# Kernel tuning notes

Measured on AMD Instinct MI355X. Metric: run time of the kernel, lower is better.

The kernel has to match this reference:

```python
import jax, jax.numpy as jnp
import numpy as np

HIDDEN = 64

def setup_inputs() -> dict:
    key = jax.random.key(0)
    ks = jax.random.split(key, 10)
    B, E = 8, 200000
    h = jax.random.normal(ks[0], (B, E, HIDDEN), dtype=jnp.float32)
    J = jax.random.normal(ks[1], (B, E, 1), dtype=jnp.float32)
    b_in = jax.random.normal(ks[2], (B, E, 1), dtype=jnp.float32)
    b_out = jax.random.normal(ks[3], (B, E, 1), dtype=jnp.float32)
    d_in = HIDDEN + 4
    # PyTorch Linear default init: U(-1/sqrt(fan_in), 1/sqrt(fan_in))
    def lin(kw, kb, fan_in, fan_out):
        bound = 1.0 / np.sqrt(fan_in)
        W = jax.random.uniform(kw, (fan_in, fan_out), minval=-bound, maxval=bound, dtype=jnp.float32)
        b = jax.random.uniform(kb, (fan_out,), minval=-bound, maxval=bound, dtype=jnp.float32)
        return W, b
    W1, b1 = lin(ks[4], ks[5], d_in, 64)
    W2, b2 = lin(ks[6], ks[7], 64, 64)
    W3, b3 = lin(ks[8], ks[9], 64, 5)
    return {"h": h, "J": J, "b_in": b_in, "b_out": b_out,
            "W1": W1, "b1": b1, "W2": W2, "b2": b2, "W3": W3, "b3": b3}

def reference(h, J, b_in, b_out, W1, b1, W2, b2, W3, b3):
    # concat order matches torch.cat((h, b_in, b_out, J, -J), 2)
    x = jnp.concatenate((h, b_in, b_out, J, -J), axis=2)  # [B,E,hidden+4]
    x = jax.nn.relu(jnp.einsum('bei,io->beo', x, W1) + b1)
    x = jax.nn.relu(jnp.einsum('bei,io->beo', x, W2) + b2)
    message = jnp.einsum('bei,io->beo', x, W3) + b3  # [B,E,5]
    return message
```

## Files before the change

### kernel.cpp

```cpp
#include <hip/hip_runtime.h>

typedef __bf16 bf16x8 __attribute__((ext_vector_type(8)));
typedef float  f32x4  __attribute__((ext_vector_type(4)));

typedef const void GV __attribute__((address_space(1)));
typedef void       LV __attribute__((address_space(3)));

#define MFMA(A, B, C) __builtin_amdgcn_mfma_f32_16x16x32_bf16((A), (B), (C), 0, 0, 0)
#define GLL(gp, lp) __builtin_amdgcn_global_load_lds((GV*)(gp), (LV*)(lp), 16, 0, 0)

__global__ __launch_bounds__(256, 2)
void msg_mlp(const float* __restrict__ hbuf, const float* __restrict__ Jbuf,
             const float* __restrict__ binb, const float* __restrict__ boutb,
             const float* __restrict__ W1, const float* __restrict__ b1,
             const float* __restrict__ W2, const float* __restrict__ b2,
             const float* __restrict__ W3, const float* __restrict__ b3,
             float* __restrict__ out, int n_rows, int n_tiles)
{
    __shared__ __align__(16) char smem[32768];
    const int lane = threadIdx.x & 63;
    const int e = lane & 15;
    const int q = lane >> 4;
    const int wv = (int)(threadIdx.x >> 6);
    const int wid = blockIdx.x * 4 + wv;
    const int nw  = gridDim.x * 4;
    char* wbase = smem + wv * 8192;

    const int o_e = 16 * (lane ^ q);
    const int o_o = 16 * (lane ^ (q + 4));
    const int X   = (e & 7) << 4;
    const int d0 = 256*e + ((64*q +  0) ^ X);
    const int d1 = 256*e + ((64*q + 16) ^ X);
    const int d2 = 256*e + ((64*q + 32) ^ X);
    const int d3 = 256*e + ((64*q + 48) ^ X);

    bf16x8 a1[4][2];
#pragma unroll
    for (int mt = 0; mt < 4; ++mt)
#pragma unroll
      for (int kk = 0; kk < 2; ++kk)
#pragma unroll
        for (int i = 0; i < 8; ++i)
          a1[mt][kk][i] = (__bf16)W1[(16*q + 8*kk + i)*64 + 16*mt + e];

    bf16x8 a1x[4];
#pragma unroll
    for (int mt = 0; mt < 4; ++mt) {
      const int o = 16*mt + e;
      float w0;
      if      (q == 0) w0 =  W1[64*64 + o];
      else if (q == 1) w0 =  W1[65*64 + o];
      else if (q == 2) w0 =  W1[66*64 + o];
      else             w0 = -W1[67*64 + o];
      a1x[mt][0] = (__bf16)w0;
      a1x[mt][1] = (q == 0) ? (__bf16)b1[o] : (__bf16)0.0f;
#pragma unroll
      for (int i = 2; i < 8; ++i) a1x[mt][i] = (__bf16)0.0f;
    }

    bf16x8 a2[4][2];
#pragma unroll
    for (int mt = 0; mt < 4; ++mt)
#pragma unroll
      for (int kk = 0; kk < 2; ++kk)
#pragma unroll
        for (int i = 0; i < 8; ++i) {
          const int f = 16*(2*kk + (i>>2)) + 4*q + (i&3);
          a2[mt][kk][i] = (__bf16)W2[f*64 + 16*mt + e];
        }
    bf16x8 a3[2];
#pragma unroll
    for (int kk = 0; kk < 2; ++kk)
#pragma unroll
      for (int i = 0; i < 8; ++i) {
        const int f = 16*(2*kk + (i>>2)) + 4*q + (i&3);
        a3[kk][i] = (e < 5) ? (__bf16)W3[f*5 + e] : (__bf16)0.0f;
      }
    float b2r[4][4];
#pragma unroll
    for (int mt = 0; mt < 4; ++mt)
#pragma unroll
      for (int r = 0; r < 4; ++r) b2r[mt][r] = b2[16*mt + 4*q + r];
    float b3r[4];
#pragma unroll
    for (int r = 0; r < 4; ++r) b3r[r] = (4*q + r < 5) ? b3[4*q + r] : 0.0f;

    const float* sptr = (q == 0) ? binb : (q == 1) ? boutb : Jbuf;
    const __bf16 biasf = (q == 0) ? (__bf16)1.0f : (__bf16)0.0f;

    auto stage = [&](int tt, char* dst) {
      const char* g = (const char*)hbuf + (size_t)tt * 4096;
      GLL(g +        o_e, dst);
      GLL(g + 1024 + o_o, dst + 1024);
      GLL(g + 2048 + o_e, dst + 2048);
      GLL(g + 3072 + o_o, dst + 3072);
    };

    int t = wid;
    if (t >= n_tiles) return;
    stage(t, wbase);
    float scur = sptr[(size_t)t * 16 + e];
    int cur = 0;

    for (; t < n_tiles; t += nw) {
      int tn = t + nw; if (tn >= n_tiles) tn = t;
      stage(tn, wbase + ((cur ^ 1) << 12));
      float snext = sptr[(size_t)tn * 16 + e];

      asm volatile("s_waitcnt vmcnt(5)" ::: "memory");

      const char* src = wbase + (cur << 12);
      const f32x4 v0 = *(const f32x4*)(src + d0);
      const f32x4 v1 = *(const f32x4*)(src + d1);
      const f32x4 v2 = *(const f32x4*)(src + d2);
      const f32x4 v3 = *(const f32x4*)(src + d3);

      bf16x8 xb0, xb1, xb2;
#pragma unroll
      for (int i = 0; i < 4; ++i) {
        xb0[i]     = (__bf16)v0[i];
        xb0[i + 4] = (__bf16)v1[i];
        xb1[i]     = (__bf16)v2[i];
        xb1[i + 4] = (__bf16)v3[i];
      }
      xb2[0] = (__bf16)scur; xb2[1] = biasf;
#pragma unroll
      for (int i = 2; i < 8; ++i) xb2[i] = (__bf16)0.0f;

      f32x4 acc1[4];
#pragma unroll
      for (int mt = 0; mt < 4; ++mt) {
        acc1[mt] = (f32x4){0.f, 0.f, 0.f, 0.f};
        acc1[mt] = MFMA(a1[mt][0], xb0, acc1[mt]);
        acc1[mt] = MFMA(a1[mt][1], xb1, acc1[mt]);
        acc1[mt] = MFMA(a1x[mt],   xb2, acc1[mt]);
      }
      bf16x8 y[2];
#pragma unroll
      for (int kk = 0; kk < 2; ++kk)
#pragma unroll
        for (int i = 0; i < 8; ++i)
          y[kk][i] = (__bf16)fmaxf(acc1[2*kk + (i>>2)][i & 3], 0.0f);

      f32x4 acc2[4];
#pragma unroll
      for (int mt = 0; mt < 4; ++mt) {
        acc2[mt] = (f32x4){b2r[mt][0], b2r[mt][1], b2r[mt][2], b2r[mt][3]};
        acc2[mt] = MFMA(a2[mt][0], y[0], acc2[mt]);
        acc2[mt] = MFMA(a2[mt][1], y[1], acc2[mt]);
      }
      bf16x8 z[2];
#pragma unroll
      for (int kk = 0; kk < 2; ++kk)
#pragma unroll
        for (int i = 0; i < 8; ++i)
          z[kk][i] = (__bf16)fmaxf(acc2[2*kk + (i>>2)][i & 3], 0.0f);

      f32x4 acc3 = (f32x4){b3r[0], b3r[1], b3r[2], b3r[3]};
      acc3 = MFMA(a3[0], z[0], acc3);
      acc3 = MFMA(a3[1], z[1], acc3);

      const int rowi = t * 16 + e;
      if (rowi < n_rows) {
        float* orow = out + (size_t)rowi * 5;
        if (q == 0) {
          orow[0] = acc3[0]; orow[1] = acc3[1];
          orow[2] = acc3[2]; orow[3] = acc3[3];
        } else if (q == 1) {
          orow[4] = acc3[0];
        }
      }
      __builtin_amdgcn_sched_barrier(0);

      scur = snext;
      cur ^= 1;
    }
}

extern "C" void kernel_launch(void* const* d_in, const int* in_sizes, int n_in,
                              void* d_out, int out_size, void* d_ws, size_t ws_size,
                              hipStream_t stream) {
    const float* h     = (const float*)d_in[0];
    const float* J     = (const float*)d_in[1];
    const float* b_in  = (const float*)d_in[2];
    const float* b_out = (const float*)d_in[3];
    const float* W1    = (const float*)d_in[4];
    const float* b1    = (const float*)d_in[5];
    const float* W2    = (const float*)d_in[6];
    const float* b2    = (const float*)d_in[7];
    const float* W3    = (const float*)d_in[8];
    const float* b3    = (const float*)d_in[9];
    float* out = (float*)d_out;

    const int n_rows  = in_sizes[1];
    const int n_tiles = (n_rows + 15) / 16;

    dim3 grid(512), block(256);
    hipLaunchKernelGGL(msg_mlp, grid, block, 0, stream,
                       h, J, b_in, b_out, W1, b1, W2, b2, W3, b3,
                       out, n_rows, n_tiles);
}
```

Baseline: 96.90 us.

## Triple-buffer LDS tile staging to deepen the global-load prefetch pipeline

Each wave's LDS region grows from two to three 4KB tile buffers. Tiles are now prefetched two iterations ahead instead of one, and the buffers rotate after each computed tile. The per-tile compute and store is moved into a lambda, and the vmcnt wait thresholds are adjusted so more loads can be in flight. The goal is to hide more HBM latency in this bandwidth-bound MLP, at the cost of 48KB of LDS per block (which may limit occupancy) and a more fragile vmcnt accounting that also counts the output stores.

```diff
diff --git a/kernel.cpp b/kernel.cpp
--- a/kernel.cpp
+++ b/kernel.cpp
@@ -17,14 +17,14 @@
              const float* __restrict__ W3, const float* __restrict__ b3,
              float* __restrict__ out, int n_rows, int n_tiles)
 {
-    __shared__ __align__(16) char smem[32768];
+    __shared__ __align__(16) char smem[49152];
     const int lane = threadIdx.x & 63;
     const int e = lane & 15;
     const int q = lane >> 4;
     const int wv = (int)(threadIdx.x >> 6);
     const int wid = blockIdx.x * 4 + wv;
     const int nw  = gridDim.x * 4;
-    char* wbase = smem + wv * 8192;
+    char* wbase = smem + wv * 12288;
 
     const int o_e = 16 * (lane ^ q);
     const int o_o = 16 * (lane ^ (q + 4));
@@ -96,20 +96,7 @@
       GLL(g + 3072 + o_o, dst + 3072);
     };
 
-    int t = wid;
-    if (t >= n_tiles) return;
-    stage(t, wbase);
-    float scur = sptr[(size_t)t * 16 + e];
-    int cur = 0;
-
-    for (; t < n_tiles; t += nw) {
-      int tn = t + nw; if (tn >= n_tiles) tn = t;
-      stage(tn, wbase + ((cur ^ 1) << 12));
-      float snext = sptr[(size_t)tn * 16 + e];
-
-      asm volatile("s_waitcnt vmcnt(5)" ::: "memory");
-
-      const char* src = wbase + (cur << 12);
+    auto compute_store = [&](const char* src, float s, int tt) {
       const f32x4 v0 = *(const f32x4*)(src + d0);
       const f32x4 v1 = *(const f32x4*)(src + d1);
       const f32x4 v2 = *(const f32x4*)(src + d2);
@@ -123,7 +110,7 @@
         xb1[i]     = (__bf16)v2[i];
         xb1[i + 4] = (__bf16)v3[i];
       }
-      xb2[0] = (__bf16)scur; xb2[1] = biasf;
+      xb2[0] = (__bf16)s; xb2[1] = biasf;
 #pragma unroll
       for (int i = 2; i < 8; ++i) xb2[i] = (__bf16)0.0f;
 
@@ -160,7 +147,7 @@
       acc3 = MFMA(a3[0], z[0], acc3);
       acc3 = MFMA(a3[1], z[1], acc3);
 
-      const int rowi = t * 16 + e;
+      const int rowi = tt * 16 + e;
       if (rowi < n_rows) {
         float* orow = out + (size_t)rowi * 5;
         if (q == 0) {
@@ -171,9 +158,36 @@
         }
       }
       __builtin_amdgcn_sched_barrier(0);
-
-      scur = snext;
-      cur ^= 1;
+    };
+
+    int t = wid;
+    if (t >= n_tiles) return;
+    const int last = n_tiles - 1;
+
+    char* bufA = wbase;
+    char* bufB = wbase + 4096;
+    char* bufC = wbase + 8192;
+
+    const int tB = (t +   nw <= last) ? t +   nw : last;
+    const int tC = (t + 2*nw <= last) ? t + 2*nw : last;
+    stage(t,  bufA); float sA = sptr[(size_t)t  * 16 + e];
+    stage(tB, bufB); float sB = sptr[(size_t)tB * 16 + e];
+    stage(tC, bufC); float sC = sptr[(size_t)tC * 16 + e];
+
+    asm volatile("s_waitcnt vmcnt(10)" ::: "memory");
+    compute_store(bufA, sA, t);
+
+    for (t += nw; t < n_tiles; t += nw) {
+      const int tp = (t + 2*nw <= last) ? t + 2*nw : last;
+      stage(tp, bufA);
+      const float sN = sptr[(size_t)tp * 16 + e];
+
+      asm volatile("s_waitcnt vmcnt(12)" ::: "memory");
+
+      compute_store(bufB, sB, t);
+
+      char* tmp = bufA; bufA = bufB; bufB = bufC; bufC = tmp;
+      sB = sC; sC = sN;
     }
 }
 
```

Measured after the change: 96.83 us. Within noise of the previous version (-0.1%).

## Move MLP weights to shared LDS, drop async double-buffering, raise occupancy

Applied to the files above, without the earlier changes.

Weight fragments and biases no longer sit in per-thread registers. They are staged once per block into LDS, with the four waves splitting the loading, and re-read from LDS every tile. This cuts VGPR pressure so launch bounds can ask for 4 blocks per CU and the grid doubles to 1024. The explicit global_load_lds double-buffered prefetch of h is replaced by direct per-lane vector global loads, so latency hiding now relies on occupancy rather than software pipelining. In exchange, each tile issues extra LDS reads for the weights.

```diff
diff --git a/kernel.cpp b/kernel.cpp
--- a/kernel.cpp
+++ b/kernel.cpp
@@ -3,13 +3,9 @@
 typedef __bf16 bf16x8 __attribute__((ext_vector_type(8)));
 typedef float  f32x4  __attribute__((ext_vector_type(4)));
 
-typedef const void GV __attribute__((address_space(1)));
-typedef void       LV __attribute__((address_space(3)));
+#define MFMA(A, B, C) __builtin_amdgcn_mfma_f32_16x16x32_bf16((A), (B), (C), 0, 0, 0)
 
-#define MFMA(A, B, C) __builtin_amdgcn_mfma_f32_16x16x32_bf16((A), (B), (C), 0, 0, 0)
-#define GLL(gp, lp) __builtin_amdgcn_global_load_lds((GV*)(gp), (LV*)(lp), 16, 0, 0)
-
-__global__ __launch_bounds__(256, 2)
+__global__ __launch_bounds__(256, 4)
 void msg_mlp(const float* __restrict__ hbuf, const float* __restrict__ Jbuf,
              const float* __restrict__ binb, const float* __restrict__ boutb,
              const float* __restrict__ W1, const float* __restrict__ b1,
@@ -17,103 +13,98 @@
              const float* __restrict__ W3, const float* __restrict__ b3,
              float* __restrict__ out, int n_rows, int n_tiles)
 {
-    __shared__ __align__(16) char smem[32768];
+    __shared__ __align__(16) char wlds[27 * 1024];
     const int lane = threadIdx.x & 63;
     const int e = lane & 15;
     const int q = lane >> 4;
     const int wv = (int)(threadIdx.x >> 6);
     const int wid = blockIdx.x * 4 + wv;
     const int nw  = gridDim.x * 4;
-    char* wbase = smem + wv * 8192;
+    char* slot = wlds + lane * 16;
 
-    const int o_e = 16 * (lane ^ q);
-    const int o_o = 16 * (lane ^ (q + 4));
-    const int X   = (e & 7) << 4;
-    const int d0 = 256*e + ((64*q +  0) ^ X);
-    const int d1 = 256*e + ((64*q + 16) ^ X);
-    const int d2 = 256*e + ((64*q + 32) ^ X);
-    const int d3 = 256*e + ((64*q + 48) ^ X);
-
-    bf16x8 a1[4][2];
+    if (wv == 0) {
 #pragma unroll
-    for (int mt = 0; mt < 4; ++mt)
+      for (int mt = 0; mt < 4; ++mt)
 #pragma unroll
-      for (int kk = 0; kk < 2; ++kk)
+        for (int kk = 0; kk < 2; ++kk) {
+          bf16x8 v;
 #pragma unroll
-        for (int i = 0; i < 8; ++i)
-          a1[mt][kk][i] = (__bf16)W1[(16*q + 8*kk + i)*64 + 16*mt + e];
-
-    bf16x8 a1x[4];
+          for (int i = 0; i < 8; ++i)
+            v[i] = (__bf16)W1[(16*q + 8*kk + i)*64 + 16*mt + e];
+          *(bf16x8*)(slot + (mt*2 + kk) * 1024) = v;
+        }
 #pragma unroll
-    for (int mt = 0; mt < 4; ++mt) {
-      const int o = 16*mt + e;
-      float w0;
-      if      (q == 0) w0 =  W1[64*64 + o];
-      else if (q == 1) w0 =  W1[65*64 + o];
-      else if (q == 2) w0 =  W1[66*64 + o];
-      else             w0 = -W1[67*64 + o];
-      a1x[mt][0] = (__bf16)w0;
-      a1x[mt][1] = (q == 0) ? (__bf16)b1[o] : (__bf16)0.0f;
+      for (int mt = 0; mt < 4; ++mt) {
+        const int o = 16*mt + e;
+        float w0;
+        if      (q == 0) w0 =  W1[64*64 + o];
+        else if (q == 1) w0 =  W1[65*64 + o];
+        else if (q == 2) w0 =  W1[66*64 + o];
+        else             w0 = -W1[67*64 + o];
+        bf16x8 v;
+        v[0] = (__bf16)w0;
+        v[1] = (q == 0) ? (__bf16)b1[o] : (__bf16)0.0f;
 #pragma unroll
-      for (int i = 2; i < 8; ++i) a1x[mt][i] = (__bf16)0.0f;
-    }
-
-    bf16x8 a2[4][2];
+        for (int i = 2; i < 8; ++i) v[i] = (__bf16)0.0f;
+        *(bf16x8*)(slot + (8 + mt) * 1024) = v;
+      }
+    } else if (wv == 1) {
 #pragma unroll
-    for (int mt = 0; mt < 4; ++mt)
+      for (int mt = 0; mt < 4; ++mt)
 #pragma unroll
-      for (int kk = 0; kk < 2; ++kk)
+        for (int kk = 0; kk < 2; ++kk) {
+          bf16x8 v;
+#pragma unroll
+          for (int i = 0; i < 8; ++i) {
+            const int f = 16*(2*kk + (i>>2)) + 4*q + (i&3);
+            v[i] = (__bf16)W2[f*64 + 16*mt + e];
+          }
+          *(bf16x8*)(slot + (12 + mt*2 + kk) * 1024) = v;
+        }
+    } else if (wv == 2) {
+#pragma unroll
+      for (int kk = 0; kk < 2; ++kk) {
+        bf16x8 v;
 #pragma unroll
         for (int i = 0; i < 8; ++i) {
           const int f = 16*(2*kk + (i>>2)) + 4*q + (i&3);
-          a2[mt][kk][i] = (__bf16)W2[f*64 + 16*mt + e];
+          v[i] = (e < 5) ? (__bf16)W3[f*5 + e] : (__bf16)0.0f;
         }
-    bf16x8 a3[2];
+        *(bf16x8*)(slot + (20 + kk) * 1024) = v;
+      }
+      f32x4 v3;
 #pragma unroll
-    for (int kk = 0; kk < 2; ++kk)
+      for (int r = 0; r < 4; ++r) v3[r] = (4*q + r < 5) ? b3[4*q + r] : 0.0f;
+      *(f32x4*)(slot + 26 * 1024) = v3;
+    } else {
 #pragma unroll
-      for (int i = 0; i < 8; ++i) {
-        const int f = 16*(2*kk + (i>>2)) + 4*q + (i&3);
-        a3[kk][i] = (e < 5) ? (__bf16)W3[f*5 + e] : (__bf16)0.0f;
+      for (int mt = 0; mt < 4; ++mt) {
+        f32x4 v;
+#pragma unroll
+        for (int r = 0; r < 4; ++r) v[r] = b2[16*mt + 4*q + r];
+        *(f32x4*)(slot + (22 + mt) * 1024) = v;
       }
-    float b2r[4][4];
-#pragma unroll
-    for (int mt = 0; mt < 4; ++mt)
-#pragma unroll
-      for (int r = 0; r < 4; ++r) b2r[mt][r] = b2[16*mt + 4*q + r];
-    float b3r[4];
-#pragma unroll
-    for (int r = 0; r < 4; ++r) b3r[r] = (4*q + r < 5) ? b3[4*q + r] : 0.0f;
+    }
 
     const float* sptr = (q == 0) ? binb : (q == 1) ? boutb : Jbuf;
     const __bf16 biasf = (q == 0) ? (__bf16)1.0f : (__bf16)0.0f;
 
-    auto stage = [&](int tt, char* dst) {
-      const char* g = (const char*)hbuf + (size_t)tt * 4096;
-      GLL(g +        o_e, dst);
-      GLL(g + 1024 + o_o, dst + 1024);
-      GLL(g + 2048 + o_e, dst + 2048);
-      GLL(g + 3072 + o_o, dst + 3072);
-    };
+    __syncthreads();
 
-    int t = wid;
-    if (t >= n_tiles) return;
-    stage(t, wbase);
-    float scur = sptr[(size_t)t * 16 + e];
-    int cur = 0;
+#pragma unroll 1
+    for (int t = wid; t < n_tiles; t += nw) {
+      int z0 = 0;
+      asm volatile("" : "+s"(z0));
+      const char* Wf = slot + z0;
 
-    for (; t < n_tiles; t += nw) {
-      int tn = t + nw; if (tn >= n_tiles) tn = t;
-      stage(tn, wbase + ((cur ^ 1) << 12));
-      float snext = sptr[(size_t)tn * 16 + e];
-
-      asm volatile("s_waitcnt vmcnt(5)" ::: "memory");
-
-      const char* src = wbase + (cur << 12);
-      const f32x4 v0 = *(const f32x4*)(src + d0);
-      const f32x4 v1 = *(const f32x4*)(src + d1);
-      const f32x4 v2 = *(const f32x4*)(src + d2);
-      const f32x4 v3 = *(const f32x4*)(src + d3);
+      int re = t * 16 + e;
+      if (re >= n_rows) re = n_rows - 1;
+      const float* hr = hbuf + (size_t)re * 64 + q * 16;
+      const f32x4 v0 = *(const f32x4*)(hr);
+      const f32x4 v1 = *(const f32x4*)(hr + 4);
+      const f32x4 v2 = *(const f32x4*)(hr + 8);
+      const f32x4 v3 = *(const f32x4*)(hr + 12);
+      const float s  = sptr[re];
 
       bf16x8 xb0, xb1, xb2;
 #pragma unroll
@@ -123,17 +114,20 @@
         xb1[i]     = (__bf16)v2[i];
         xb1[i + 4] = (__bf16)v3[i];
       }
-      xb2[0] = (__bf16)scur; xb2[1] = biasf;
+      xb2[0] = (__bf16)s; xb2[1] = biasf;
 #pragma unroll
       for (int i = 2; i < 8; ++i) xb2[i] = (__bf16)0.0f;
 
       f32x4 acc1[4];
 #pragma unroll
       for (int mt = 0; mt < 4; ++mt) {
+        const bf16x8 wa = *(const bf16x8*)(Wf + (mt*2 + 0) * 1024);
+        const bf16x8 wb = *(const bf16x8*)(Wf + (mt*2 + 1) * 1024);
+        const bf16x8 wx = *(const bf16x8*)(Wf + (8 + mt)  * 1024);
         acc1[mt] = (f32x4){0.f, 0.f, 0.f, 0.f};
-        acc1[mt] = MFMA(a1[mt][0], xb0, acc1[mt]);
-        acc1[mt] = MFMA(a1[mt][1], xb1, acc1[mt]);
-        acc1[mt] = MFMA(a1x[mt],   xb2, acc1[mt]);
+        acc1[mt] = MFMA(wa, xb0, acc1[mt]);
+        acc1[mt] = MFMA(wb, xb1, acc1[mt]);
+        acc1[mt] = MFMA(wx, xb2, acc1[mt]);
       }
       bf16x8 y[2];
 #pragma unroll
@@ -145,9 +139,11 @@
       f32x4 acc2[4];
 #pragma unroll
       for (int mt = 0; mt < 4; ++mt) {
-        acc2[mt] = (f32x4){b2r[mt][0], b2r[mt][1], b2r[mt][2], b2r[mt][3]};
-        acc2[mt] = MFMA(a2[mt][0], y[0], acc2[mt]);
-        acc2[mt] = MFMA(a2[mt][1], y[1], acc2[mt]);
+        const bf16x8 wa = *(const bf16x8*)(Wf + (12 + mt*2 + 0) * 1024);
+        const bf16x8 wb = *(const bf16x8*)(Wf + (12 + mt*2 + 1) * 1024);
+        acc2[mt] = *(const f32x4*)(Wf + (22 + mt) * 1024);
+        acc2[mt] = MFMA(wa, y[0], acc2[mt]);
+        acc2[mt] = MFMA(wb, y[1], acc2[mt]);
       }
       bf16x8 z[2];
 #pragma unroll
@@ -156,9 +152,9 @@
         for (int i = 0; i < 8; ++i)
           z[kk][i] = (__bf16)fmaxf(acc2[2*kk + (i>>2)][i & 3], 0.0f);
 
-      f32x4 acc3 = (f32x4){b3r[0], b3r[1], b3r[2], b3r[3]};
-      acc3 = MFMA(a3[0], z[0], acc3);
-      acc3 = MFMA(a3[1], z[1], acc3);
+      f32x4 acc3 = *(const f32x4*)(Wf + 26 * 1024);
+      acc3 = MFMA(*(const bf16x8*)(Wf + 20 * 1024), z[0], acc3);
+      acc3 = MFMA(*(const bf16x8*)(Wf + 21 * 1024), z[1], acc3);
 
       const int rowi = t * 16 + e;
       if (rowi < n_rows) {
@@ -170,10 +166,6 @@
           orow[4] = acc3[0];
         }
       }
-      __builtin_amdgcn_sched_barrier(0);
-
-      scur = snext;
-      cur ^= 1;
     }
 }
 
@@ -195,7 +187,7 @@
     const int n_rows  = in_sizes[1];
     const int n_tiles = (n_rows + 15) / 16;
 
-    dim3 grid(512), block(256);
+    dim3 grid(1024), block(256);
     hipLaunchKernelGGL(msg_mlp, grid, block, 0, stream,
                        h, J, b_in, b_out, W1, b1, W2, b2, W3, b3,
                        out, n_rows, n_tiles);
```

Measured after the change: 92.55 us, median of 2. 1.05x faster.
